# Kernel optimization log

Hardware: AMD Instinct MI355X
Metric: run time of the kernel (lower is better)

The kernel has to match this reference:

```python
import jax, jax.numpy as jnp
import numpy as np

B, GH, GW = 64, 14, 14
H = 512   # features_len == lstm hidden size == lstm_len
E = 512   # embedding_len
A = 512   # attention_len
V = 10000 # wordmap_len
MAXCAP = 50


def setup_inputs() -> dict:
    key = jax.random.key(0)
    ks = jax.random.split(key, 12)
    s = 0.02
    caplens = jax.random.randint(ks[2], (B, 1), 2, MAXCAP + 1, jnp.int32)
    caplens = caplens.at[0, 0].set(MAXCAP)  # ensure max(decode_lengths) == MAXCAP-1 (static T)
    return dict(
        image_features=jax.random.normal(ks[0], (B, GH, GW, H), jnp.float32),
        caps=jax.random.randint(ks[1], (B, MAXCAP), 0, V, jnp.int32),
        caplens=caplens,
        emb_table=jax.random.normal(ks[3], (V, E), jnp.float32) * s,
        W_ih=jax.random.normal(ks[4], (4 * H, E + H), jnp.float32) * s,
        W_hh=jax.random.normal(ks[5], (4 * H, H), jnp.float32) * s,
        b_ih=jnp.zeros((4 * H,), jnp.float32),
        b_hh=jnp.zeros((4 * H,), jnp.float32),
        W_enc=jax.random.normal(ks[6], (A, H), jnp.float32) * s,
        b_enc=jnp.zeros((A,), jnp.float32),
        W_dec=jax.random.normal(ks[7], (A, H), jnp.float32) * s,
        b_dec=jnp.zeros((A,), jnp.float32),
        W_full=jax.random.normal(ks[8], (1, A), jnp.float32) * s,
        b_full=jnp.zeros((1,), jnp.float32),
        W_score=jax.random.normal(ks[9], (V, H), jnp.float32) * s,
        b_score=jnp.zeros((V,), jnp.float32),
    )


def _forward(image_features, emb_table, W_ih, W_hh, b_ih, b_hh,
             W_enc, b_enc, W_dec, b_dec, W_full, b_full, W_score, b_score,
             caps, caplens):
    Bsz = image_features.shape[0]
    feats = image_features.reshape(Bsz, -1, image_features.shape[-1])  # (B, P, H)
    cl = caplens[:, 0]
    sort_ind = jnp.argsort(-cl)                      # descending sort by caption length
    cl = cl[sort_ind]
    feats = feats[sort_ind]
    caps_s = caps[sort_ind]
    decode_lengths = cl - 1
    T = caps.shape[1] - 1                            # static; setup guarantees max(decode_lengths)==T
    emb = emb_table[caps_s]                          # (B, MAXCAP, E)
    enc_att = jnp.einsum('bph,ah->bpa', feats, W_enc) + b_enc  # precomputed encoder attention proj
    mask = jnp.arange(T)[None, :] < decode_lengths[:, None]    # (B, T): row active at step t

    h0 = jnp.zeros((Bsz, feats.shape[-1]), feats.dtype)
    c0 = jnp.zeros_like(h0)

    def step(carry, xs):
        h, c = carry
        emb_t, m_t = xs                              # (B,E), (B,)
        # attention (show-attend-tell style)
        att2 = h @ W_dec.T + b_dec                   # (B, A)
        e = jnp.einsum('bpa,a->bp', jax.nn.relu(enc_att + att2[:, None, :]), W_full[0]) + b_full[0]
        alpha = jax.nn.softmax(e, axis=-1)           # (B, P)
        ctx = jnp.einsum('bp,bph->bh', alpha, feats) # (B, H)
        # LSTMCell
        x = jnp.concatenate([emb_t, ctx], axis=1)    # (B, E+H)
        gates = x @ W_ih.T + b_ih + h @ W_hh.T + b_hh
        i, f, g, o = jnp.split(gates, 4, axis=1)
        c_new = jax.nn.sigmoid(f) * c + jax.nn.sigmoid(i) * jnp.tanh(g)
        h_new = jax.nn.sigmoid(o) * jnp.tanh(c_new)
        score = h_new @ W_score.T + b_score          # (B, V)
        m = m_t[:, None]
        # rows past their decode length keep stale state and write zeros (matches :k slicing)
        h = jnp.where(m, h_new, h)
        c = jnp.where(m, c_new, c)
        return (h, c), (jnp.where(m, score, jnp.zeros((), score.dtype)),
                        jnp.where(m, alpha, jnp.zeros((), alpha.dtype)))

    (_, _), (scores, weights) = jax.lax.scan(
        step, (h0, c0), (emb[:, :T, :].transpose(1, 0, 2), mask.T))
    scores = scores.transpose(1, 0, 2)   # (B, T, V)
    weights = weights.transpose(1, 0, 2) # (B, T, P)
    return scores, caps_s, decode_lengths, weights, sort_ind


def reference(image_features, caps, caplens, emb_table, W_ih, W_hh, b_ih, b_hh,
              W_enc, b_enc, W_dec, b_dec, W_full, b_full, W_score, b_score):
    return _forward(image_features, emb_table, W_ih, W_hh, b_ih, b_hh,
                    W_enc, b_enc, W_dec, b_dec, W_full, b_full, W_score, b_score,
                    caps, caplens)
```

## Files before the change

kernel.cpp:

```cpp
#include <hip/hip_runtime.h>
#include <math.h>


#define WS_SORT   0
#define WS_DL     64
#define WS_NB     128
#define WS_ROWOFF 192
#define WS_CAPS   256
#define WS_RMAP   3456
#define WS_H      6592
#define WS_C      39360
#define WS_ATT2   72128
#define WS_E      104896
#define WS_Z      117696
#define WS_CTXP   117952
#define WS_PG     249024
#define WS_HALL   2346176
#define WS_ENC    3951808

#define OUT_SCORES 0
#define OUT_CAPS   31360000
#define OUT_DL     31363200
#define OUT_W      31363264
#define OUT_SORT   31977920

#define LSW 196

__device__ __forceinline__ float sigm(float x) { return 1.f / (1.f + expf(-x)); }

__device__ __forceinline__ float4 f4add(float4 a, float4 b) {
  return make_float4(a.x + b.x, a.y + b.y, a.z + b.z, a.w + b.w);
}

__device__ __forceinline__ int swz128(int m) { return (m >> 3) * 12 + (m & 7); }

__device__ __forceinline__ void stage128_strided(const float* __restrict__ src, int row0, int ld, int k0,
                                                 float* __restrict__ dst, int tid, int nrows_valid) {
#pragma unroll
  for (int i = 0; i < 2; ++i) {
    int lin = tid + 256 * i;
    int m = lin >> 2, kf = lin & 3;
    float4 v = make_float4(0.f, 0.f, 0.f, 0.f);
    if (m < nrows_valid) v = *(const float4*)(src + (long)(row0 + m) * ld + k0 + kf * 4);
    int mc = swz128(m);
    dst[(kf * 4 + 0) * LSW + mc] = v.x;
    dst[(kf * 4 + 1) * LSW + mc] = v.y;
    dst[(kf * 4 + 2) * LSW + mc] = v.z;
    dst[(kf * 4 + 3) * LSW + mc] = v.w;
  }
}

__device__ __forceinline__ void stage128_gather(const float* __restrict__ src, const int* __restrict__ bases,
                                                int k0, float* __restrict__ dst, int tid) {
#pragma unroll
  for (int i = 0; i < 2; ++i) {
    int lin = tid + 256 * i;
    int m = lin >> 2, kf = lin & 3;
    float4 v = *(const float4*)(src + bases[m] + k0 + kf * 4);
    int mc = swz128(m);
    dst[(kf * 4 + 0) * LSW + mc] = v.x;
    dst[(kf * 4 + 1) * LSW + mc] = v.y;
    dst[(kf * 4 + 2) * LSW + mc] = v.z;
    dst[(kf * 4 + 3) * LSW + mc] = v.w;
  }
}

__device__ __forceinline__ void gemm_acc128(const float* __restrict__ As, const float* __restrict__ Bs,
                                            float acc[8][8], int tx, int ty) {
#pragma unroll
  for (int kk = 0; kk < 16; ++kk) {
    const float4* ar = (const float4*)(As + kk * LSW + tx * 12);
    const float4* br = (const float4*)(Bs + kk * LSW + ty * 12);
    float4 a0 = ar[0], a1 = ar[1];
    float4 b0 = br[0], b1 = br[1];
    float av[8] = {a0.x, a0.y, a0.z, a0.w, a1.x, a1.y, a1.z, a1.w};
    float bv[8] = {b0.x, b0.y, b0.z, b0.w, b1.x, b1.y, b1.z, b1.w};
#pragma unroll
    for (int i = 0; i < 8; ++i)
#pragma unroll
      for (int j = 0; j < 8; ++j)
        acc[i][j] = fmaf(av[i], bv[j], acc[i][j]);
  }
}

__global__ __launch_bounds__(64) void setup_kernel(const int* __restrict__ caps, const int* __restrict__ caplens,
                                                   float* __restrict__ ws, float* __restrict__ out) {
  __shared__ int cl_s[64], so_s[64], dl_s[64], nb_s[49], ro_s[50];
  int i = threadIdx.x;
  cl_s[i] = caplens[i];
  __syncthreads();
  int cli = cl_s[i];
  int r = 0;
  for (int j = 0; j < 64; ++j) {
    int clj = cl_s[j];
    r += (clj > cli) || (clj == cli && j < i);
  }
  so_s[r] = i;
  dl_s[r] = cli - 1;
  __syncthreads();
  int* iws = (int*)ws;
  iws[WS_SORT + i] = so_s[i];
  iws[WS_DL + i] = dl_s[i];
  out[OUT_SORT + i] = (float)so_s[i];
  out[OUT_DL + i] = (float)dl_s[i];
  if (i < 49) {
    int n = 0;
    for (int b = 0; b < 64; ++b) n += (dl_s[b] > i);
    iws[WS_NB + i] = n;
    nb_s[i] = n;
  }
  __syncthreads();
  if (i == 0) {
    int acc = 0;
    for (int t = 0; t < 49; ++t) { ro_s[t] = acc; acc += nb_s[t]; }
    ro_s[49] = acc;
    iws[WS_NB + 49] = acc;
  }
  __syncthreads();
  if (i < 50) iws[WS_ROWOFF + i] = ro_s[i];
  int R = ro_s[49];
  for (int rr = i; rr < 3136; rr += 64) {
    int val = 0;
    if (rr < R) {
      int t = 0;
      while (t < 48 && ro_s[t + 1] <= rr) ++t;
      val = t * 64 + (rr - ro_s[t]);
    }
    iws[WS_RMAP + rr] = val;
  }
  for (int j = i; j < 3200; j += 64) {
    int k = j / 50, jj = j - k * 50;
    int cv = caps[so_s[k] * 50 + jj];
    iws[WS_CAPS + j] = cv;
    out[OUT_CAPS + j] = (float)cv;
  }
}

__global__ void zero_init_kernel(float* __restrict__ out, float* __restrict__ ws, const float* __restrict__ b_dec) {
  const float4 z = make_float4(0.f, 0.f, 0.f, 0.f);
  float4* out4 = (float4*)out;
  float4* ws4 = (float4*)ws;
  const float4* bd4 = (const float4*)b_dec;
  for (long idx = (long)blockIdx.x * 256 + threadIdx.x; idx < 8018240L; idx += (long)gridDim.x * 256) {
    if (idx < 7840000L) {
      out4[idx] = z;
    } else if (idx < 7993664L) {
      out4[7840816L + (idx - 7840000L)] = z;
    } else if (idx < 8010048L) {
      ws4[1648L + (idx - 7993664L)] = z;
    } else {
      long j = idx - 8010048L;
      ws4[18032L + j] = bd4[j & 127];
    }
  }
}

__global__ __launch_bounds__(256) void encatt_kernel(const float* __restrict__ image, const float* __restrict__ W_enc,
                                                     const float* __restrict__ b_enc, float* __restrict__ ws) {
  __shared__ __align__(16) float As[16 * LSW];
  __shared__ __align__(16) float Bs[16 * LSW];
  __shared__ int rb[128];
  int tid = threadIdx.x;
  const int* iws = (const int*)ws;
  int mt = blockIdx.x, nt = blockIdx.y;
  if (tid < 128) {
    int r = mt * 128 + tid;
    int b = r / 196;
    int p = r - b * 196;
    rb[tid] = iws[WS_SORT + b] * 100352 + p * 512;
  }
  float acc[8][8] = {};
  for (int ch = 0; ch < 32; ++ch) {
    __syncthreads();
    stage128_gather(image, rb, ch * 16, As, tid);
    stage128_strided(W_enc, nt * 128, 512, ch * 16, Bs, tid, 128);
    __syncthreads();
    gemm_acc128(As, Bs, acc, tid & 15, tid >> 4);
  }
  int tx = tid & 15, ty = tid >> 4;
  int r0 = mt * 128 + tx * 8;
  int n0 = nt * 128 + ty * 8;
#pragma unroll
  for (int i = 0; i < 8; ++i) {
    float* cp = ws + WS_ENC + (long)(r0 + i) * 512 + n0;
    *(float4*)(cp)     = make_float4(acc[i][0] + b_enc[n0],     acc[i][1] + b_enc[n0 + 1],
                                     acc[i][2] + b_enc[n0 + 2], acc[i][3] + b_enc[n0 + 3]);
    *(float4*)(cp + 4) = make_float4(acc[i][4] + b_enc[n0 + 4], acc[i][5] + b_enc[n0 + 5],
                                     acc[i][6] + b_enc[n0 + 6], acc[i][7] + b_enc[n0 + 7]);
  }
}

__global__ __launch_bounds__(512) void ectx_kernel(float* __restrict__ ws, const float* __restrict__ image,
                                                   const float* __restrict__ W_full, const float* __restrict__ b_full,
                                                   int t) {
  const int* iws = (const int*)ws;
  int b = blockIdx.x;
  if (b >= iws[WS_NB + t]) return;
  int pg = blockIdx.y;
  __shared__ float att2_s[512], wf_s[512], e_s[52];
  int tid = threadIdx.x;
  att2_s[tid] = ws[WS_ATT2 + b * 512 + tid];
  wf_s[tid] = W_full[tid];
  __syncthreads();
  int w = tid >> 6, lane = tid & 63;
  float bf0 = b_full[0];
  for (int idx = w; idx < 49; idx += 8) {
    int p = pg * 49 + idx;
    const float* er = ws + WS_ENC + (long)(b * 196 + p) * 512;
    float acc = 0.f;
#pragma unroll
    for (int a8 = 0; a8 < 8; ++a8) {
      int a = (a8 << 6) + lane;
      float v = er[a] + att2_s[a];
      acc = fmaf(fmaxf(v, 0.f), wf_s[a], acc);
    }
#pragma unroll
    for (int off = 32; off; off >>= 1) acc += __shfl_down(acc, off);
    if (lane == 0) e_s[idx] = expf(acc + bf0);
  }
  __syncthreads();
  if (tid < 49) ws[WS_E + b * 200 + pg * 49 + tid] = e_s[tid];
  if (tid == 0) {
    float zz = 0.f;
    for (int j = 0; j < 49; ++j) zz += e_s[j];
    ws[WS_Z + pg * 64 + b] = zz;
  }
  long sb = (long)iws[WS_SORT + b] * 100352;
  float a0 = 0.f;
  for (int j = 0; j < 49; ++j) {
    a0 = fmaf(e_s[j], image[sb + (long)(pg * 49 + j) * 512 + tid], a0);
  }
  ws[WS_CTXP + pg * 32768 + b * 512 + tid] = a0;
}

__global__ __launch_bounds__(256) void gates_kernel(float* __restrict__ ws, const float* __restrict__ emb,
                                                    const float* __restrict__ W_ih, const float* __restrict__ W_hh,
                                                    int t) {
  __shared__ __align__(16) float As[96 * 68];
  __shared__ __align__(16) float Bs[96 * 68];
  __shared__ int rbe[64];
  __shared__ float rcpz_s[64];
  int tid = threadIdx.x;
  int nt = blockIdx.x;
  int ks = blockIdx.y;
  int* iws = (int*)ws;
  if (tid < 64) {
    rbe[tid] = iws[WS_CAPS + tid * 50 + t] * 512;
    float zz = ws[WS_Z + tid] + ws[WS_Z + 64 + tid] + ws[WS_Z + 128 + tid] + ws[WS_Z + 192 + tid];
    rcpz_s[tid] = 1.f / zz;
  }
  __syncthreads();
#pragma unroll
  for (int c = 0; c < 3; ++c) {
    int k0 = ks * 96 + c * 32;
#pragma unroll
    for (int i = 0; i < 2; ++i) {
      int lin = tid + 256 * i;
      int kf = lin >> 6;
      int m = lin & 63;
      float4 v;
      if (k0 < 512) {
        v = *(const float4*)(emb + (long)rbe[m] + k0 + kf * 4);
      } else if (k0 < 1024) {
        const float* base = ws + WS_CTXP + m * 512 + (k0 - 512) + kf * 4;
        float4 v0 = *(const float4*)(base);
        float4 v1 = *(const float4*)(base + 32768);
        float4 v2 = *(const float4*)(base + 65536);
        float4 v3 = *(const float4*)(base + 98304);
        float rz = rcpz_s[m];
        v = make_float4((v0.x + v1.x + v2.x + v3.x) * rz, (v0.y + v1.y + v2.y + v3.y) * rz,
                        (v0.z + v1.z + v2.z + v3.z) * rz, (v0.w + v1.w + v2.w + v3.w) * rz);
      } else {
        v = *(const float4*)(ws + WS_H + m * 512 + (k0 - 1024) + kf * 4);
      }
      float* da = As + (c * 32 + kf * 4) * 68 + m;
      da[0] = v.x; da[68] = v.y; da[136] = v.z; da[204] = v.w;
      const float* srcB = (k0 < 1024) ? (W_ih + (long)(nt * 64 + m) * 1024 + k0 + kf * 4)
                                      : (W_hh + (long)(nt * 64 + m) * 512 + (k0 - 1024) + kf * 4);
      float4 bv = *(const float4*)srcB;
      float* db = Bs + (c * 32 + kf * 4) * 68 + m;
      db[0] = bv.x; db[68] = bv.y; db[136] = bv.z; db[204] = bv.w;
    }
  }
  __syncthreads();
  int w = tid >> 6, lane = tid & 63;
  int tx = lane & 7, ty = lane >> 3;
  float acc[8][2] = {};
#pragma unroll 8
  for (int kk = 0; kk < 96; ++kk) {
    const float4* ar = (const float4*)(As + kk * 68 + tx * 8);
    float4 a0 = ar[0], a1 = ar[1];
    float2 bv = *(const float2*)(Bs + kk * 68 + w * 16 + ty * 2);
    float av[8] = {a0.x, a0.y, a0.z, a0.w, a1.x, a1.y, a1.z, a1.w};
#pragma unroll
    for (int i = 0; i < 8; ++i) {
      acc[i][0] = fmaf(av[i], bv.x, acc[i][0]);
      acc[i][1] = fmaf(av[i], bv.y, acc[i][1]);
    }
  }
  float* pg = ws + WS_PG + ks * 131072;
  int j0 = nt * 64 + w * 16 + ty * 2;
#pragma unroll
  for (int i = 0; i < 8; ++i) {
    int b = tx * 8 + i;
    *(float2*)(pg + b * 2048 + j0) = make_float2(acc[i][0], acc[i][1]);
  }
}

__global__ __launch_bounds__(512) void lstm_att2_kernel(float* __restrict__ ws, const float* __restrict__ b_ih,
                                                        const float* __restrict__ b_hh, const float* __restrict__ W_dec,
                                                        const float* __restrict__ b_dec, float* __restrict__ out, int t) {
  const int* iws = (const int*)ws;
  int b = blockIdx.x;
  int as = blockIdx.y;
  int hh = threadIdx.x;
  int nb = iws[WS_NB + t];
  __shared__ float h_s[512], red[512];
  float gi = b_ih[hh] + b_hh[hh];
  float gf = b_ih[512 + hh] + b_hh[512 + hh];
  float gg = b_ih[1024 + hh] + b_hh[1024 + hh];
  float go = b_ih[1536 + hh] + b_hh[1536 + hh];
  const float* pgp = ws + WS_PG + b * 2048;
#pragma unroll
  for (int ks = 0; ks < 16; ++ks) {
    const float* p = pgp + ks * 131072;
    gi += p[hh]; gf += p[512 + hh]; gg += p[1024 + hh]; go += p[1536 + hh];
  }
  float c = ws[WS_C + b * 512 + hh];
  float cn = sigm(gf) * c + sigm(gi) * tanhf(gg);
  float hn = sigm(go) * tanhf(cn);
  h_s[hh] = hn;
  if (b < nb) {
    if (as == 0) {
      ws[WS_C + b * 512 + hh] = cn;
      ws[WS_H + b * 512 + hh] = hn;
      ws[WS_HALL + (long)(iws[WS_ROWOFF + t] + b) * 512 + hh] = hn;
    }
    if (hh < 49) {
      float zz = ws[WS_Z + b] + ws[WS_Z + 64 + b] + ws[WS_Z + 128 + b] + ws[WS_Z + 192 + b];
      int p = as * 49 + hh;
      out[OUT_W + (long)(b * 49 + t) * 196 + p] = ws[WS_E + b * 200 + p] / zz;
    }
  }
  __syncthreads();
  int a = as * 128 + (hh >> 2);
  int part = hh & 3;
  const float* wd = W_dec + (long)a * 512 + part * 128;
  const float* hp = h_s + part * 128;
  float s = 0.f;
#pragma unroll 8
  for (int j = 0; j < 32; ++j) {
    float4 wv = *(const float4*)(wd + 4 * j);
    s = fmaf(hp[4 * j], wv.x, s);
    s = fmaf(hp[4 * j + 1], wv.y, s);
    s = fmaf(hp[4 * j + 2], wv.z, s);
    s = fmaf(hp[4 * j + 3], wv.w, s);
  }
  red[hh] = s;
  __syncthreads();
  if (part == 0) {
    float v = red[hh] + red[hh + 1] + red[hh + 2] + red[hh + 3] + b_dec[a];
    ws[WS_ATT2 + b * 512 + a] = v;
  }
}

__global__ __launch_bounds__(256) void score_kernel(const float* __restrict__ ws, const float* __restrict__ W_score,
                                                    const float* __restrict__ b_score, float* __restrict__ out) {
  __shared__ __align__(16) float As[16 * LSW];
  __shared__ __align__(16) float Bs[16 * LSW];
  const int* iws = (const int*)ws;
  int mt = blockIdx.x, nt = blockIdx.y;
  int R = iws[WS_NB + 49];
  if (mt * 128 >= R) return;
  int tid = threadIdx.x;
  int mvalid = R - mt * 128; if (mvalid > 128) mvalid = 128;
  int nvalid = 10000 - nt * 128; if (nvalid > 128) nvalid = 128;
  float acc[8][8] = {};
  for (int ch = 0; ch < 32; ++ch) {
    __syncthreads();
    stage128_strided(ws + WS_HALL, mt * 128, 512, ch * 16, As, tid, mvalid);
    stage128_strided(W_score, nt * 128, 512, ch * 16, Bs, tid, nvalid);
    __syncthreads();
    gemm_acc128(As, Bs, acc, tid & 15, tid >> 4);
  }
  int tx = tid & 15, ty = tid >> 4;
  int n0 = nt * 128 + ty * 8;
#pragma unroll
  for (int i = 0; i < 8; ++i) {
    int r = mt * 128 + tx * 8 + i;
    if (r >= R) continue;
    int tb = iws[WS_RMAP + r];
    int bb = tb & 63, tt = tb >> 6;
    float* cp = out + (long)bb * 490000 + tt * 10000 + n0;
    if (n0 + 4 <= 10000)
      *(float4*)(cp)     = make_float4(acc[i][0] + b_score[n0],     acc[i][1] + b_score[n0 + 1],
                                       acc[i][2] + b_score[n0 + 2], acc[i][3] + b_score[n0 + 3]);
    if (n0 + 8 <= 10000)
      *(float4*)(cp + 4) = make_float4(acc[i][4] + b_score[n0 + 4], acc[i][5] + b_score[n0 + 5],
                                       acc[i][6] + b_score[n0 + 6], acc[i][7] + b_score[n0 + 7]);
  }
}

extern "C" void kernel_launch(void* const* d_in, const int* in_sizes, int n_in,
                              void* d_out, int out_size, void* d_ws, size_t ws_size,
                              hipStream_t stream) {
  const float* image   = (const float*)d_in[0];
  const int*   caps    = (const int*)d_in[1];
  const int*   caplens = (const int*)d_in[2];
  const float* emb     = (const float*)d_in[3];
  const float* W_ih    = (const float*)d_in[4];
  const float* W_hh    = (const float*)d_in[5];
  const float* b_ih    = (const float*)d_in[6];
  const float* b_hh    = (const float*)d_in[7];
  const float* W_enc   = (const float*)d_in[8];
  const float* b_enc   = (const float*)d_in[9];
  const float* W_dec   = (const float*)d_in[10];
  const float* b_dec   = (const float*)d_in[11];
  const float* W_full  = (const float*)d_in[12];
  const float* b_full  = (const float*)d_in[13];
  const float* W_score = (const float*)d_in[14];
  const float* b_score = (const float*)d_in[15];
  float* out = (float*)d_out;
  float* ws  = (float*)d_ws;

  setup_kernel<<<1, 64, 0, stream>>>(caps, caplens, ws, out);
  zero_init_kernel<<<2048, 256, 0, stream>>>(out, ws, b_dec);
  encatt_kernel<<<dim3(98, 4), 256, 0, stream>>>(image, W_enc, b_enc, ws);
  for (int t = 0; t < 49; ++t) {
    ectx_kernel<<<dim3(64, 4), 512, 0, stream>>>(ws, image, W_full, b_full, t);
    gates_kernel<<<dim3(32, 16), 256, 0, stream>>>(ws, emb, W_ih, W_hh, t);
    lstm_att2_kernel<<<dim3(64, 4), 512, 0, stream>>>(ws, b_ih, b_hh, W_dec, b_dec, out, t);
  }
  score_kernel<<<dim3(25, 79), 256, 0, stream>>>(ws, W_score, b_score, out);
}
```

Measured before the change: 2.378 ms.

## Rework per-step kernels: vectorized attention, 8x8 gates microtile, early-exit LSTM

The ectx kernel now keeps the attention and W_full values in registers, reads them with float4 loads, and computes the context with four row groups that are reduced through shared memory. The gates GEMM drops from 256 to 64 threads per block, with an 8x8 register microtile over chunked K tiles. The LSTM kernel returns early for inactive rows and reads the gate partial sums as float4 through shared memory. The aim is to cut per-step latency from memory traffic and instruction count, at the cost of lower occupancy in the gates kernel.

```diff
diff --git a/kernel.cpp b/kernel.cpp
--- a/kernel.cpp
+++ b/kernel.cpp
@@ -24,6 +24,8 @@
 #define OUT_W      31363264
 #define OUT_SORT   31977920
 
+#define KC  32
+#define LST 68
 #define LSW 196
 
 __device__ __forceinline__ float sigm(float x) { return 1.f / (1.f + expf(-x)); }
@@ -33,6 +35,53 @@
 }
 
 __device__ __forceinline__ int swz128(int m) { return (m >> 3) * 12 + (m & 7); }
+
+__device__ __forceinline__ void gemm_acc(const float* __restrict__ As, const float* __restrict__ Bs,
+                                         float acc[8][8], int tx, int ty) {
+#pragma unroll 8
+  for (int kk = 0; kk < KC; ++kk) {
+    const float4* ar = (const float4*)(As + kk * LST + tx * 8);
+    const float4* br = (const float4*)(Bs + kk * LST + ty * 8);
+    float4 a0 = ar[0], a1 = ar[1];
+    float4 b0 = br[0], b1 = br[1];
+    float av[8] = {a0.x, a0.y, a0.z, a0.w, a1.x, a1.y, a1.z, a1.w};
+    float bv[8] = {b0.x, b0.y, b0.z, b0.w, b1.x, b1.y, b1.z, b1.w};
+#pragma unroll
+    for (int i = 0; i < 8; ++i)
+#pragma unroll
+      for (int j = 0; j < 8; ++j)
+        acc[i][j] = fmaf(av[i], bv[j], acc[i][j]);
+  }
+}
+
+__device__ __forceinline__ void load_tile_strided(const float* __restrict__ src, int row0, int ld, int k0,
+                                                  float* __restrict__ dst, int tid, int nrows_valid) {
+#pragma unroll
+  for (int i = 0; i < 8; ++i) {
+    int lin = tid + 64 * i;
+    int m = lin >> 3, kf = lin & 7;
+    float4 v = make_float4(0.f, 0.f, 0.f, 0.f);
+    if (m < nrows_valid) v = *(const float4*)(src + (long)(row0 + m) * ld + k0 + kf * 4);
+    dst[(kf * 4 + 0) * LST + m] = v.x;
+    dst[(kf * 4 + 1) * LST + m] = v.y;
+    dst[(kf * 4 + 2) * LST + m] = v.z;
+    dst[(kf * 4 + 3) * LST + m] = v.w;
+  }
+}
+
+__device__ __forceinline__ void load_tile_gather(const float* __restrict__ src, const int* __restrict__ bases,
+                                                 int k0, float* __restrict__ dst, int tid) {
+#pragma unroll
+  for (int i = 0; i < 8; ++i) {
+    int lin = tid + 64 * i;
+    int m = lin >> 3, kf = lin & 7;
+    float4 v = *(const float4*)(src + bases[m] + k0 + kf * 4);
+    dst[(kf * 4 + 0) * LST + m] = v.x;
+    dst[(kf * 4 + 1) * LST + m] = v.y;
+    dst[(kf * 4 + 2) * LST + m] = v.z;
+    dst[(kf * 4 + 3) * LST + m] = v.w;
+  }
+}
 
 __device__ __forceinline__ void stage128_strided(const float* __restrict__ src, int row0, int ld, int k0,
                                                  float* __restrict__ dst, int tid, int nrows_valid) {
@@ -197,113 +246,115 @@
   int b = blockIdx.x;
   if (b >= iws[WS_NB + t]) return;
   int pg = blockIdx.y;
-  __shared__ float att2_s[512], wf_s[512], e_s[52];
+  __shared__ float e_s[64];
+  __shared__ __align__(16) float ctxp_s[2048];
   int tid = threadIdx.x;
-  att2_s[tid] = ws[WS_ATT2 + b * 512 + tid];
-  wf_s[tid] = W_full[tid];
-  __syncthreads();
   int w = tid >> 6, lane = tid & 63;
+
+  float4 at0 = *(const float4*)(ws + WS_ATT2 + b * 512 + lane * 4);
+  float4 at1 = *(const float4*)(ws + WS_ATT2 + b * 512 + 256 + lane * 4);
+  float4 wf0 = *(const float4*)(W_full + lane * 4);
+  float4 wf1 = *(const float4*)(W_full + 256 + lane * 4);
   float bf0 = b_full[0];
+
   for (int idx = w; idx < 49; idx += 8) {
-    int p = pg * 49 + idx;
-    const float* er = ws + WS_ENC + (long)(b * 196 + p) * 512;
-    float acc = 0.f;
-#pragma unroll
-    for (int a8 = 0; a8 < 8; ++a8) {
-      int a = (a8 << 6) + lane;
-      float v = er[a] + att2_s[a];
-      acc = fmaf(fmaxf(v, 0.f), wf_s[a], acc);
-    }
+    const float* er = ws + WS_ENC + (long)(b * 196 + pg * 49 + idx) * 512;
+    float4 e0 = *(const float4*)(er + lane * 4);
+    float4 e1 = *(const float4*)(er + 256 + lane * 4);
+    float acc = fmaxf(e0.x + at0.x, 0.f) * wf0.x + fmaxf(e0.y + at0.y, 0.f) * wf0.y +
+                fmaxf(e0.z + at0.z, 0.f) * wf0.z + fmaxf(e0.w + at0.w, 0.f) * wf0.w +
+                fmaxf(e1.x + at1.x, 0.f) * wf1.x + fmaxf(e1.y + at1.y, 0.f) * wf1.y +
+                fmaxf(e1.z + at1.z, 0.f) * wf1.z + fmaxf(e1.w + at1.w, 0.f) * wf1.w;
 #pragma unroll
     for (int off = 32; off; off >>= 1) acc += __shfl_down(acc, off);
     if (lane == 0) e_s[idx] = expf(acc + bf0);
   }
   __syncthreads();
   if (tid < 49) ws[WS_E + b * 200 + pg * 49 + tid] = e_s[tid];
-  if (tid == 0) {
-    float zz = 0.f;
-    for (int j = 0; j < 49; ++j) zz += e_s[j];
-    ws[WS_Z + pg * 64 + b] = zz;
+  if (tid < 64) {
+    float zv = (tid < 49) ? e_s[tid] : 0.f;
+#pragma unroll
+    for (int off = 32; off; off >>= 1) zv += __shfl_down(zv, off);
+    if (tid == 0) ws[WS_Z + pg * 64 + b] = zv;
   }
   long sb = (long)iws[WS_SORT + b] * 100352;
-  float a0 = 0.f;
-  for (int j = 0; j < 49; ++j) {
-    a0 = fmaf(e_s[j], image[sb + (long)(pg * 49 + j) * 512 + tid], a0);
-  }
-  ws[WS_CTXP + pg * 32768 + b * 512 + tid] = a0;
-}
-
-__global__ __launch_bounds__(256) void gates_kernel(float* __restrict__ ws, const float* __restrict__ emb,
-                                                    const float* __restrict__ W_ih, const float* __restrict__ W_hh,
-                                                    int t) {
-  __shared__ __align__(16) float As[96 * 68];
-  __shared__ __align__(16) float Bs[96 * 68];
+  int rg = tid >> 7, l1 = tid & 127;
+  float4 a = make_float4(0.f, 0.f, 0.f, 0.f);
+  for (int idx = rg; idx < 49; idx += 4) {
+    float al = e_s[idx];
+    float4 v = *(const float4*)(image + sb + (long)(pg * 49 + idx) * 512 + l1 * 4);
+    a.x = fmaf(al, v.x, a.x); a.y = fmaf(al, v.y, a.y);
+    a.z = fmaf(al, v.z, a.z); a.w = fmaf(al, v.w, a.w);
+  }
+  *(float4*)(ctxp_s + rg * 512 + l1 * 4) = a;
+  __syncthreads();
+  if (tid < 128) {
+    float4 v0 = *(const float4*)(ctxp_s + tid * 4);
+    float4 v1 = *(const float4*)(ctxp_s + 512 + tid * 4);
+    float4 v2 = *(const float4*)(ctxp_s + 1024 + tid * 4);
+    float4 v3 = *(const float4*)(ctxp_s + 1536 + tid * 4);
+    *(float4*)(ws + WS_CTXP + pg * 32768 + b * 512 + tid * 4) =
+        make_float4(v0.x + v1.x + v2.x + v3.x, v0.y + v1.y + v2.y + v3.y,
+                    v0.z + v1.z + v2.z + v3.z, v0.w + v1.w + v2.w + v3.w);
+  }
+}
+
+__global__ __launch_bounds__(64) void gates_kernel(float* __restrict__ ws, const float* __restrict__ emb,
+                                                   const float* __restrict__ W_ih, const float* __restrict__ W_hh,
+                                                   int t) {
+  __shared__ __align__(16) float As[KC * LST];
+  __shared__ __align__(16) float Bs[KC * LST];
   __shared__ int rbe[64];
   __shared__ float rcpz_s[64];
   int tid = threadIdx.x;
   int nt = blockIdx.x;
   int ks = blockIdx.y;
   int* iws = (int*)ws;
-  if (tid < 64) {
-    rbe[tid] = iws[WS_CAPS + tid * 50 + t] * 512;
+  rbe[tid] = iws[WS_CAPS + tid * 50 + t] * 512;
+  {
     float zz = ws[WS_Z + tid] + ws[WS_Z + 64 + tid] + ws[WS_Z + 128 + tid] + ws[WS_Z + 192 + tid];
     rcpz_s[tid] = 1.f / zz;
   }
-  __syncthreads();
-#pragma unroll
-  for (int c = 0; c < 3; ++c) {
-    int k0 = ks * 96 + c * 32;
-#pragma unroll
-    for (int i = 0; i < 2; ++i) {
-      int lin = tid + 256 * i;
-      int kf = lin >> 6;
-      int m = lin & 63;
-      float4 v;
-      if (k0 < 512) {
-        v = *(const float4*)(emb + (long)rbe[m] + k0 + kf * 4);
-      } else if (k0 < 1024) {
-        const float* base = ws + WS_CTXP + m * 512 + (k0 - 512) + kf * 4;
+  float acc[8][8] = {};
+  for (int ch = 0; ch < 3; ++ch) {
+    int k0 = ks * 96 + ch * 32;
+    __syncthreads();
+    if (k0 < 512) {
+      load_tile_gather(emb, rbe, k0, As, tid);
+    } else if (k0 < 1024) {
+      int kc = k0 - 512;
+#pragma unroll
+      for (int i = 0; i < 8; ++i) {
+        int lin = tid + 64 * i;
+        int m = lin >> 3, kf = lin & 7;
+        const float* base = ws + WS_CTXP + m * 512 + kc + kf * 4;
         float4 v0 = *(const float4*)(base);
         float4 v1 = *(const float4*)(base + 32768);
         float4 v2 = *(const float4*)(base + 65536);
         float4 v3 = *(const float4*)(base + 98304);
         float rz = rcpz_s[m];
-        v = make_float4((v0.x + v1.x + v2.x + v3.x) * rz, (v0.y + v1.y + v2.y + v3.y) * rz,
-                        (v0.z + v1.z + v2.z + v3.z) * rz, (v0.w + v1.w + v2.w + v3.w) * rz);
-      } else {
-        v = *(const float4*)(ws + WS_H + m * 512 + (k0 - 1024) + kf * 4);
+        As[(kf * 4 + 0) * LST + m] = (v0.x + v1.x + v2.x + v3.x) * rz;
+        As[(kf * 4 + 1) * LST + m] = (v0.y + v1.y + v2.y + v3.y) * rz;
+        As[(kf * 4 + 2) * LST + m] = (v0.z + v1.z + v2.z + v3.z) * rz;
+        As[(kf * 4 + 3) * LST + m] = (v0.w + v1.w + v2.w + v3.w) * rz;
       }
-      float* da = As + (c * 32 + kf * 4) * 68 + m;
-      da[0] = v.x; da[68] = v.y; da[136] = v.z; da[204] = v.w;
-      const float* srcB = (k0 < 1024) ? (W_ih + (long)(nt * 64 + m) * 1024 + k0 + kf * 4)
-                                      : (W_hh + (long)(nt * 64 + m) * 512 + (k0 - 1024) + kf * 4);
-      float4 bv = *(const float4*)srcB;
-      float* db = Bs + (c * 32 + kf * 4) * 68 + m;
-      db[0] = bv.x; db[68] = bv.y; db[136] = bv.z; db[204] = bv.w;
+    } else {
+      load_tile_strided(ws + WS_H, 0, 512, k0 - 1024, As, tid, 64);
     }
-  }
-  __syncthreads();
-  int w = tid >> 6, lane = tid & 63;
-  int tx = lane & 7, ty = lane >> 3;
-  float acc[8][2] = {};
-#pragma unroll 8
-  for (int kk = 0; kk < 96; ++kk) {
-    const float4* ar = (const float4*)(As + kk * 68 + tx * 8);
-    float4 a0 = ar[0], a1 = ar[1];
-    float2 bv = *(const float2*)(Bs + kk * 68 + w * 16 + ty * 2);
-    float av[8] = {a0.x, a0.y, a0.z, a0.w, a1.x, a1.y, a1.z, a1.w};
-#pragma unroll
-    for (int i = 0; i < 8; ++i) {
-      acc[i][0] = fmaf(av[i], bv.x, acc[i][0]);
-      acc[i][1] = fmaf(av[i], bv.y, acc[i][1]);
-    }
-  }
+    if (k0 < 1024) load_tile_strided(W_ih, nt * 64, 1024, k0, Bs, tid, 64);
+    else           load_tile_strided(W_hh, nt * 64, 512, k0 - 1024, Bs, tid, 64);
+    __syncthreads();
+    gemm_acc(As, Bs, acc, tid & 7, tid >> 3);
+  }
+  int tx = tid & 7, ty = tid >> 3;
   float* pg = ws + WS_PG + ks * 131072;
-  int j0 = nt * 64 + w * 16 + ty * 2;
+  int j0 = nt * 64 + ty * 8;
 #pragma unroll
   for (int i = 0; i < 8; ++i) {
     int b = tx * 8 + i;
-    *(float2*)(pg + b * 2048 + j0) = make_float2(acc[i][0], acc[i][1]);
+    float* cp = pg + b * 2048 + j0;
+    *(float4*)(cp)     = make_float4(acc[i][0], acc[i][1], acc[i][2], acc[i][3]);
+    *(float4*)(cp + 4) = make_float4(acc[i][4], acc[i][5], acc[i][6], acc[i][7]);
   }
 }
 
@@ -312,35 +363,35 @@
                                                         const float* __restrict__ b_dec, float* __restrict__ out, int t) {
   const int* iws = (const int*)ws;
   int b = blockIdx.x;
+  if (b >= iws[WS_NB + t]) return;
   int as = blockIdx.y;
   int hh = threadIdx.x;
-  int nb = iws[WS_NB + t];
+  __shared__ __align__(16) float g[2048];
   __shared__ float h_s[512], red[512];
-  float gi = b_ih[hh] + b_hh[hh];
-  float gf = b_ih[512 + hh] + b_hh[512 + hh];
-  float gg = b_ih[1024 + hh] + b_hh[1024 + hh];
-  float go = b_ih[1536 + hh] + b_hh[1536 + hh];
-  const float* pgp = ws + WS_PG + b * 2048;
+  const float4* bi4 = (const float4*)b_ih;
+  const float4* bh4 = (const float4*)b_hh;
+  float4 A = f4add(bi4[hh], bh4[hh]);
+  const float* pgb = ws + WS_PG + b * 2048;
 #pragma unroll
   for (int ks = 0; ks < 16; ++ks) {
-    const float* p = pgp + ks * 131072;
-    gi += p[hh]; gf += p[512 + hh]; gg += p[1024 + hh]; go += p[1536 + hh];
-  }
+    A = f4add(A, *(const float4*)(pgb + (long)ks * 131072 + hh * 4));
+  }
+  *(float4*)(g + hh * 4) = A;
+  __syncthreads();
+  float gi = g[hh], gf = g[512 + hh], gg = g[1024 + hh], go = g[1536 + hh];
   float c = ws[WS_C + b * 512 + hh];
   float cn = sigm(gf) * c + sigm(gi) * tanhf(gg);
   float hn = sigm(go) * tanhf(cn);
   h_s[hh] = hn;
-  if (b < nb) {
-    if (as == 0) {
-      ws[WS_C + b * 512 + hh] = cn;
-      ws[WS_H + b * 512 + hh] = hn;
-      ws[WS_HALL + (long)(iws[WS_ROWOFF + t] + b) * 512 + hh] = hn;
-    }
-    if (hh < 49) {
-      float zz = ws[WS_Z + b] + ws[WS_Z + 64 + b] + ws[WS_Z + 128 + b] + ws[WS_Z + 192 + b];
-      int p = as * 49 + hh;
-      out[OUT_W + (long)(b * 49 + t) * 196 + p] = ws[WS_E + b * 200 + p] / zz;
-    }
+  if (as == 0) {
+    ws[WS_C + b * 512 + hh] = cn;
+    ws[WS_H + b * 512 + hh] = hn;
+    ws[WS_HALL + (long)(iws[WS_ROWOFF + t] + b) * 512 + hh] = hn;
+  }
+  if (hh < 49) {
+    float zz = ws[WS_Z + b] + ws[WS_Z + 64 + b] + ws[WS_Z + 128 + b] + ws[WS_Z + 192 + b];
+    int p = as * 49 + hh;
+    out[OUT_W + (long)(b * 49 + t) * 196 + p] = ws[WS_E + b * 200 + p] / zz;
   }
   __syncthreads();
   int a = as * 128 + (hh >> 2);
@@ -428,7 +479,7 @@
   encatt_kernel<<<dim3(98, 4), 256, 0, stream>>>(image, W_enc, b_enc, ws);
   for (int t = 0; t < 49; ++t) {
     ectx_kernel<<<dim3(64, 4), 512, 0, stream>>>(ws, image, W_full, b_full, t);
-    gates_kernel<<<dim3(32, 16), 256, 0, stream>>>(ws, emb, W_ih, W_hh, t);
+    gates_kernel<<<dim3(32, 16), 64, 0, stream>>>(ws, emb, W_ih, W_hh, t);
     lstm_att2_kernel<<<dim3(64, 4), 512, 0, stream>>>(ws, b_ih, b_hh, W_dec, b_dec, out, t);
   }
   score_kernel<<<dim3(25, 79), 256, 0, stream>>>(ws, W_score, b_score, out);
```

Result: slower. 2.616 ms (+10.0%).
